# Performance work log

Measured on AMD Instinct MI355X. Metric: run time of the kernel, lower is better.

## Reference

```python
import jax, jax.numpy as jnp
import numpy as np

B, N, D_NODE, D_EDGE, D_GRAPH = 2, 1024, 128, 16, 128
MID, OUT = 64, 128


def _linear_params(key, fan_in, fan_out):
    # haiku Linear default: truncated-normal(stddev=1/sqrt(fan_in)) weight, zero bias
    w = jax.random.normal(key, (fan_in, fan_out), dtype=jnp.float32) / np.sqrt(fan_in)
    b = jnp.zeros((fan_out,), dtype=jnp.float32)
    return w, b


def setup_inputs() -> dict:
    key = jax.random.key(0)
    ks = jax.random.split(key, 12)
    features = jax.random.normal(ks[0], (B, N, D_NODE), dtype=jnp.float32)
    e_features = jax.random.normal(ks[1], (B, N, N, D_EDGE), dtype=jnp.float32)
    g_features = jax.random.normal(ks[2], (B, D_GRAPH), dtype=jnp.float32)
    adj = jax.random.randint(ks[3], (B, N, N), 0, 2).astype(jnp.float32)
    # ensure self-loops so every row has at least one valid neighbor
    adj = jnp.maximum(adj, jnp.eye(N, dtype=jnp.float32)[None])
    Wm, bm = _linear_params(ks[4], D_NODE, OUT)
    Wskip, bskip = _linear_params(ks[5], D_NODE, OUT)
    W1, b1 = _linear_params(ks[6], D_NODE, MID)
    W2, b2 = _linear_params(ks[7], D_NODE, MID)
    We, be = _linear_params(ks[8], D_EDGE, MID)
    Wg, bg = _linear_params(ks[9], D_GRAPH, MID)
    Wa, ba = _linear_params(ks[10], MID, 1)
    return dict(features=features, e_features=e_features, g_features=g_features,
                adj=adj, Wm=Wm, bm=bm, Wskip=Wskip, bskip=bskip,
                W1=W1, b1=b1, W2=W2, b2=b2, We=We, be=be, Wg=Wg, bg=bg,
                Wa=Wa, ba=ba)


def reference(features, e_features, g_features, adj,
              Wm, bm, Wskip, bskip, W1, b1, W2, b2, We, be, Wg, bg, Wa, ba):
    # bias mask: 0 where edge exists, -1e9 where not
    bias_mat = (adj - 1.0) * 1e9  # (b,n,n)

    values = features @ Wm + bm          # (b,n,out)
    pre_att_1 = features @ W1 + b1       # (b,n,mid) -> per-target j
    pre_att_2 = features @ W2 + b2       # (b,n,mid) -> per-source i
    pre_att_e = e_features @ We + be     # (b,n,n,mid)
    pre_att_g = g_features @ Wg + bg     # (b,mid)

    # pre_att[b,i,j] = p1[b,j] + p2[b,i] + pe[b,i,j] + pg[b]
    pre_att = (pre_att_1[:, None, :, :] + pre_att_2[:, :, None, :]
               + pre_att_e + pre_att_g[:, None, None, :])  # (b,n,n,mid)

    logits = jnp.squeeze(jax.nn.leaky_relu(pre_att) @ Wa + ba, axis=-1)  # (b,n,n)
    coefs = jax.nn.softmax(logits + bias_mat, axis=-1)                   # (b,n,n)

    ret = jnp.matmul(coefs, values)       # (b,n,out)
    ret = ret + (features @ Wskip + bskip)  # residual
    return jax.nn.relu(ret)               # activation=relu
```

## Files before the change

kernel.cpp:

```cpp
#include <hip/hip_runtime.h>
#include <hip/hip_bf16.h>
#include <cstdint>

#define B_   2
#define N_   1024
#define DN_  128
#define DE_  16
#define DG_  128
#define MID_ 64
#define OUT_ 128
#define TI_  2
#define PR_ROWS 4

typedef short bf16x8 __attribute__((ext_vector_type(8)));
typedef float f32x4  __attribute__((ext_vector_type(4)));

__device__ inline short f2bf(float f) {
    union { float f; unsigned u; } v; v.f = f;
    unsigned r = v.u + 0x7FFFu + ((v.u >> 16) & 1u);
    return (short)(unsigned short)(r >> 16);
}

__device__ inline unsigned pk2(float lo, float hi) {
    union { __hip_bfloat162 h; unsigned u; } p;
    p.h = __float22bfloat162_rn(make_float2(lo, hi));
    return p.u;
}

__global__ void __launch_bounds__(384) prep_all(
    const float* __restrict__ features, const float* __restrict__ g_features,
    const float* __restrict__ Wm, const float* __restrict__ bm,
    const float* __restrict__ Wskip, const float* __restrict__ bskip,
    const float* __restrict__ W1, const float* __restrict__ b1,
    const float* __restrict__ W2, const float* __restrict__ b2,
    const float* __restrict__ We, const float* __restrict__ be,
    const float* __restrict__ Wg, const float* __restrict__ bg,
    float* __restrict__ values, float* __restrict__ skipo,
    float* __restrict__ P1xT, float* __restrict__ p2,
    float* __restrict__ pg, short* __restrict__ We_frag)
{
    const int t   = threadIdx.x;
    const int blk = blockIdx.x;

    if (blk == 512) {
        for (int e = t; e < 4 * 64 * 8; e += 384) {
            const int c    = e >> 9;
            const int lane = (e >> 3) & 63;
            const int j    = e & 7;
            const int quad = lane >> 4, s = lane & 15;
            short v = 0;
            if (quad < 2) v = f2bf(We[(quad * 8 + j) * MID_ + c * 16 + s]);
            We_frag[e] = v;
        }
        return;
    }
    if (blk == 513) {
        if (t < MID_) {
            float a0 = bg[t], a1 = bg[t];
            for (int k = 0; k < DG_; ++k) {
                const float w = Wg[k * MID_ + t];
                a0 += g_features[k] * w;
                a1 += g_features[DG_ + k] * w;
            }
            pg[t] = a0; pg[MID_ + t] = a1;
        }
        return;
    }

    const int r0 = blk * PR_ROWS;
    __shared__ float feat[PR_ROWS][DN_];
    for (int idx = t; idx < PR_ROWS * DN_; idx += 384)
        feat[idx >> 7][idx & 127] = features[(size_t)r0 * DN_ + idx];
    __syncthreads();

    const float* W; int c, stride; float base; float* outp; int ostride;
    if (t < 128) {
        W = Wm;    c = t;       stride = OUT_; base = bm[c];
        outp = values + (size_t)r0 * OUT_ + c; ostride = OUT_;
    } else if (t < 256) {
        W = Wskip; c = t - 128; stride = OUT_; base = bskip[c];
        outp = skipo + (size_t)r0 * OUT_ + c;  ostride = OUT_;
    } else if (t < 320) {
        W = W1;    c = t - 256; stride = MID_; base = b1[c] + be[c];
        outp = P1xT + (size_t)c * (B_ * N_) + r0; ostride = 1;
    } else {
        W = W2;    c = t - 320; stride = MID_; base = b2[c];
        outp = p2 + (size_t)r0 * MID_ + c;     ostride = MID_;
    }

    float acc[PR_ROWS] = {};
    for (int k = 0; k < DN_; ++k) {
        const float w = W[k * stride + c];
        #pragma unroll
        for (int q = 0; q < PR_ROWS; ++q) acc[q] += feat[q][k] * w;
    }
    #pragma unroll
    for (int q = 0; q < PR_ROWS; ++q) outp[q * ostride] = acc[q] + base;
}

__global__ void __launch_bounds__(256) k_logits(
    const float* __restrict__ e_features, const short* __restrict__ We_frag,
    const float* __restrict__ Wa, const float* __restrict__ P1xT,
    const float* __restrict__ p2, const float* __restrict__ pg,
    float* __restrict__ lg)
{
    const int t    = threadIdx.x;
    const int wv   = t >> 6;
    const int l    = t & 63;
    const int quad = l >> 4;
    const int s    = l & 15;
    const int r    = blockIdx.x;
    const int jb   = r & 1;
    const int ri   = r >> 1;
    const int b    = ri >> 9;
    const int i0   = (ri & 511) * TI_;

    bf16x8 bfr[4];
    float  wa_l[4][4];
    f32x4  p2l[TI_][4];
    #pragma unroll
    for (int c = 0; c < 4; ++c) {
        bfr[c] = *(const bf16x8*)&We_frag[(c * 64 + l) * 8];
        #pragma unroll
        for (int rr = 0; rr < 4; ++rr)
            wa_l[c][rr] = Wa[c * 16 + quad * 4 + rr];
        const float4 pg4 = *(const float4*)&pg[b * MID_ + c * 16 + quad * 4];
        #pragma unroll
        for (int ii = 0; ii < TI_; ++ii) {
            const float4 p4 = *(const float4*)&p2[((size_t)(b * N_ + i0 + ii)) * MID_ + c * 16 + quad * 4];
            p2l[ii][c][0] = p4.x + pg4.x;
            p2l[ii][c][1] = p4.y + pg4.y;
            p2l[ii][c][2] = p4.z + pg4.z;
            p2l[ii][c][3] = p4.w + pg4.w;
        }
    }
    const size_t erow0 = (size_t)(b * N_ + i0) * N_;
    const int jt0 = jb * 32;
    const float* p1b = P1xT + (size_t)(quad * 4) * (B_ * N_) + b * N_ + s;

    float4 eA0[TI_][2], eA1[TI_][2];
    float  bA[4][4], bB[4][4];
    if (quad < 2) {
        #pragma unroll
        for (int ii = 0; ii < TI_; ++ii) {
            const float* ep0 = &e_features[(erow0 + (size_t)ii * N_ + (jt0 + wv) * 16 + s) * DE_ + quad * 8];
            eA0[ii][0] = *(const float4*)ep0;
            eA0[ii][1] = *(const float4*)(ep0 + 4);
            const float* ep1 = &e_features[(erow0 + (size_t)ii * N_ + (jt0 + wv + 4) * 16 + s) * DE_ + quad * 8];
            eA1[ii][0] = *(const float4*)ep1;
            eA1[ii][1] = *(const float4*)(ep1 + 4);
        }
    }
    {
        const float* pb = p1b + (jt0 + wv) * 16;
        #pragma unroll
        for (int c = 0; c < 4; ++c)
            #pragma unroll
            for (int rr = 0; rr < 4; ++rr)
                bA[c][rr] = pb[(size_t)(c * 16 + rr) * (B_ * N_)];
    }

    auto do_tile = [&](float4 (&eAr)[TI_][2], float (&bC)[4][4], float (&bN)[4][4], int it) {
        const int tile = jt0 + wv + it * 4;
        const int j0   = tile * 16;

        unsigned af[TI_][4];
        #pragma unroll
        for (int ii = 0; ii < TI_; ++ii) {
            if (quad < 2) {
                af[ii][0] = pk2(eAr[ii][0].x, eAr[ii][0].y);
                af[ii][1] = pk2(eAr[ii][0].z, eAr[ii][0].w);
                af[ii][2] = pk2(eAr[ii][1].x, eAr[ii][1].y);
                af[ii][3] = pk2(eAr[ii][1].z, eAr[ii][1].w);
            } else {
                af[ii][0] = af[ii][1] = af[ii][2] = af[ii][3] = 0u;
            }
        }
        if (it < 6 && quad < 2) {
            #pragma unroll
            for (int ii = 0; ii < TI_; ++ii) {
                const float* ep = &e_features[(erow0 + (size_t)ii * N_ + (size_t)(tile + 8) * 16 + s) * DE_ + quad * 8];
                eAr[ii][0] = *(const float4*)ep;
                eAr[ii][1] = *(const float4*)(ep + 4);
            }
        }
        if (it < 7) {
            const float* pb = p1b + (tile + 4) * 16;
            #pragma unroll
            for (int c = 0; c < 4; ++c)
                #pragma unroll
                for (int rr = 0; rr < 4; ++rr)
                    bN[c][rr] = pb[(size_t)(c * 16 + rr) * (B_ * N_)];
        }
        #pragma unroll
        for (int ii = 0; ii < TI_; ++ii) {
            union { unsigned u[4]; bf16x8 v; } a;
            a.u[0] = af[ii][0]; a.u[1] = af[ii][1];
            a.u[2] = af[ii][2]; a.u[3] = af[ii][3];
            f32x4 acc[4];
            #pragma unroll
            for (int c = 0; c < 4; ++c)
                acc[c] = __builtin_amdgcn_mfma_f32_16x16x32_bf16(bfr[c], a.v, p2l[ii][c], 0, 0, 0);
            float part = 0.f;
            #pragma unroll
            for (int c = 0; c < 4; ++c)
                #pragma unroll
                for (int rr = 0; rr < 4; ++rr) {
                    float x = acc[c][rr] + bC[c][rr];
                    x = fmaxf(x, 0.01f * x);
                    part += x * wa_l[c][rr];
                }
            part += __shfl_xor(part, 16);
            part += __shfl_xor(part, 32);
            if (l < 16)
                lg[((size_t)(b * N_ + i0 + ii)) * N_ + j0 + l] = part;
        }
    };
    for (int it2 = 0; it2 < 8; it2 += 2) {
        do_tile(eA0, bA, bB, it2);
        do_tile(eA1, bB, bA, it2 + 1);
    }
}

__global__ void __launch_bounds__(256) k_attn(
    const float* __restrict__ lg, const float* __restrict__ adj,
    const float* __restrict__ values, const float* __restrict__ skipo,
    float* __restrict__ out)
{
    const int t  = threadIdx.x;
    const int wv = t >> 6;
    const int l  = t & 63;
    const int r  = blockIdx.x;
    const int b  = (r >> 2) & 1;
    const int i0 = (((r >> 3) << 2) | (r & 3)) * TI_;

    __shared__ float lgP[TI_][N_];
    __shared__ float redv[4][16][20];
    __shared__ float sinv[TI_];
    __shared__ float pmax[4];
    __shared__ float psum[4];

    {
        const int rw = wv & 1, h = wv >> 1;
        const int c0 = h * 512 + l * 4;
        const float* lrow = &lg[(size_t)(b * N_ + i0 + rw) * N_];
        const size_t arb  = (size_t)(b * N_ + i0 + rw) * N_;
        float4 lv[2], av[2];
        #pragma unroll
        for (int q = 0; q < 2; ++q) {
            lv[q] = *(const float4*)&lrow[c0 + 256 * q];
            av[q] = *(const float4*)&adj[arb + c0 + 256 * q];
        }
        const float NEG = -3.4e38f;
        float m = NEG;
        #pragma unroll
        for (int q = 0; q < 2; ++q) {
            m = fmaxf(m, av[q].x > 0.f ? lv[q].x : NEG);
            m = fmaxf(m, av[q].y > 0.f ? lv[q].y : NEG);
            m = fmaxf(m, av[q].z > 0.f ? lv[q].z : NEG);
            m = fmaxf(m, av[q].w > 0.f ? lv[q].w : NEG);
        }
        #pragma unroll
        for (int o = 1; o < 64; o <<= 1) m = fmaxf(m, __shfl_xor(m, o));
        if (l == 0) pmax[wv] = m;
        __syncthreads();
        m = fmaxf(pmax[rw], pmax[2 + rw]);
        float sum = 0.f;
        #pragma unroll
        for (int q = 0; q < 2; ++q) {
            float4 e4;
            e4.x = av[q].x > 0.f ? __expf(lv[q].x - m) : 0.f;
            e4.y = av[q].y > 0.f ? __expf(lv[q].y - m) : 0.f;
            e4.z = av[q].z > 0.f ? __expf(lv[q].z - m) : 0.f;
            e4.w = av[q].w > 0.f ? __expf(lv[q].w - m) : 0.f;
            *(float4*)&lgP[rw][c0 + 256 * q] = e4;
            sum += (e4.x + e4.y) + (e4.z + e4.w);
        }
        #pragma unroll
        for (int o = 1; o < 64; o <<= 1) sum += __shfl_xor(sum, o);
        if (l == 0) psum[wv] = sum;
        __syncthreads();
        if (t < TI_) sinv[t] = 1.0f / (psum[t] + psum[t + 2]);
    }

    const int cg = l & 15, jp = l >> 4, ch0 = cg * 8;
    float acc[TI_][8] = {};
    const float* vb = values + (size_t)b * N_ * OUT_ + ch0;
    for (int k = 0; k < 64; ++k) {
        const int j = wv * 4 + jp + k * 16;
        float cw[TI_];
        #pragma unroll
        for (int ii = 0; ii < TI_; ++ii) cw[ii] = lgP[ii][j];
        const float* vp = vb + (size_t)j * OUT_;
        const float4 v0 = *(const float4*)vp;
        const float4 v1 = *(const float4*)(vp + 4);
        const float vv[8] = {v0.x, v0.y, v0.z, v0.w, v1.x, v1.y, v1.z, v1.w};
        #pragma unroll
        for (int ii = 0; ii < TI_; ++ii)
            #pragma unroll
            for (int kk = 0; kk < 8; ++kk)
                acc[ii][kk] += cw[ii] * vv[kk];
    }
    #pragma unroll
    for (int ii = 0; ii < TI_; ++ii)
        #pragma unroll
        for (int kk = 0; kk < 8; ++kk) {
            acc[ii][kk] += __shfl_xor(acc[ii][kk], 16);
            acc[ii][kk] += __shfl_xor(acc[ii][kk], 32);
        }
    if (l < 16) {
        #pragma unroll
        for (int ii = 0; ii < TI_; ++ii)
            #pragma unroll
            for (int q = 0; q < 2; ++q) {
                float4 w4 = make_float4(acc[ii][q * 4], acc[ii][q * 4 + 1],
                                        acc[ii][q * 4 + 2], acc[ii][q * 4 + 3]);
                *(float4*)&redv[wv][l][ii * 8 + q * 4] = w4;
            }
    }
    __syncthreads();
    {
        const int ch = t & 127, g = ch >> 3, kk = ch & 7;
        const int ii = t >> 7;
        float sum = redv[0][g][ii * 8 + kk];
        #pragma unroll
        for (int w = 1; w < 4; ++w) sum += redv[w][g][ii * 8 + kk];
        const size_t ob = ((size_t)(b * N_ + i0 + ii)) * OUT_ + ch;
        out[ob] = fmaxf(sum * sinv[ii] + skipo[ob], 0.f);
    }
}

extern "C" void kernel_launch(void* const* d_in, const int* in_sizes, int n_in,
                              void* d_out, int out_size, void* d_ws, size_t ws_size,
                              hipStream_t stream) {
    const float* features   = (const float*)d_in[0];
    const float* e_features = (const float*)d_in[1];
    const float* g_features = (const float*)d_in[2];
    const float* adj        = (const float*)d_in[3];
    const float* Wm    = (const float*)d_in[4];
    const float* bm    = (const float*)d_in[5];
    const float* Wskip = (const float*)d_in[6];
    const float* bskip = (const float*)d_in[7];
    const float* W1    = (const float*)d_in[8];
    const float* b1    = (const float*)d_in[9];
    const float* W2    = (const float*)d_in[10];
    const float* b2    = (const float*)d_in[11];
    const float* We    = (const float*)d_in[12];
    const float* be    = (const float*)d_in[13];
    const float* Wg    = (const float*)d_in[14];
    const float* bg    = (const float*)d_in[15];
    const float* Wa    = (const float*)d_in[16];
    float* out = (float*)d_out;

    float* ws      = (float*)d_ws;
    float* values  = ws;
    float* skipo   = ws + 262144;
    float* P1xT    = ws + 524288;
    float* p2      = ws + 655360;
    float* pg      = ws + 786432;
    short* We_frag = (short*)(ws + 786560);
    float* lg      = ws + 787584;

    prep_all<<<B_ * N_ / PR_ROWS + 2, 384, 0, stream>>>(
        features, g_features, Wm, bm, Wskip, bskip, W1, b1, W2, b2,
        We, be, Wg, bg, values, skipo, P1xT, p2, pg, We_frag);
    k_logits<<<B_ * N_ / TI_ * 2, 256, 0, stream>>>(
        e_features, We_frag, Wa, P1xT, p2, pg, lg);
    k_attn<<<B_ * N_ / TI_, 256, 0, stream>>>(
        lg, adj, values, skipo, out);
}
```

Baseline: 294.9 us.

## Store P1 row-major for vector loads and triple-buffer edge feature prefetch

```diff
diff --git a/kernel.cpp b/kernel.cpp
--- a/kernel.cpp
+++ b/kernel.cpp
@@ -36,7 +36,7 @@
     const float* __restrict__ We, const float* __restrict__ be,
     const float* __restrict__ Wg, const float* __restrict__ bg,
     float* __restrict__ values, float* __restrict__ skipo,
-    float* __restrict__ P1xT, float* __restrict__ p2,
+    float* __restrict__ P1x, float* __restrict__ p2,
     float* __restrict__ pg, short* __restrict__ We_frag)
 {
     const int t   = threadIdx.x;
@@ -82,7 +82,7 @@
         outp = skipo + (size_t)r0 * OUT_ + c;  ostride = OUT_;
     } else if (t < 320) {
         W = W1;    c = t - 256; stride = MID_; base = b1[c] + be[c];
-        outp = P1xT + (size_t)c * (B_ * N_) + r0; ostride = 1;
+        outp = P1x + (size_t)r0 * MID_ + c;    ostride = MID_;
     } else {
         W = W2;    c = t - 320; stride = MID_; base = b2[c];
         outp = p2 + (size_t)r0 * MID_ + c;     ostride = MID_;
@@ -100,7 +100,7 @@
 
 __global__ void __launch_bounds__(256) k_logits(
     const float* __restrict__ e_features, const short* __restrict__ We_frag,
-    const float* __restrict__ Wa, const float* __restrict__ P1xT,
+    const float* __restrict__ Wa, const float* __restrict__ P1x,
     const float* __restrict__ p2, const float* __restrict__ pg,
     float* __restrict__ lg)
 {
@@ -116,14 +116,12 @@
     const int i0   = (ri & 511) * TI_;
 
     bf16x8 bfr[4];
-    float  wa_l[4][4];
+    float4 wa4[4];
     f32x4  p2l[TI_][4];
     #pragma unroll
     for (int c = 0; c < 4; ++c) {
         bfr[c] = *(const bf16x8*)&We_frag[(c * 64 + l) * 8];
-        #pragma unroll
-        for (int rr = 0; rr < 4; ++rr)
-            wa_l[c][rr] = Wa[c * 16 + quad * 4 + rr];
+        wa4[c] = *(const float4*)&Wa[c * 16 + quad * 4];
         const float4 pg4 = *(const float4*)&pg[b * MID_ + c * 16 + quad * 4];
         #pragma unroll
         for (int ii = 0; ii < TI_; ++ii) {
@@ -136,31 +134,36 @@
     }
     const size_t erow0 = (size_t)(b * N_ + i0) * N_;
     const int jt0 = jb * 32;
-    const float* p1b = P1xT + (size_t)(quad * 4) * (B_ * N_) + b * N_ + s;
-
-    float4 eA0[TI_][2], eA1[TI_][2];
-    float  bA[4][4], bB[4][4];
-    if (quad < 2) {
-        #pragma unroll
-        for (int ii = 0; ii < TI_; ++ii) {
-            const float* ep0 = &e_features[(erow0 + (size_t)ii * N_ + (jt0 + wv) * 16 + s) * DE_ + quad * 8];
-            eA0[ii][0] = *(const float4*)ep0;
-            eA0[ii][1] = *(const float4*)(ep0 + 4);
-            const float* ep1 = &e_features[(erow0 + (size_t)ii * N_ + (jt0 + wv + 4) * 16 + s) * DE_ + quad * 8];
-            eA1[ii][0] = *(const float4*)ep1;
-            eA1[ii][1] = *(const float4*)(ep1 + 4);
-        }
-    }
-    {
-        const float* pb = p1b + (jt0 + wv) * 16;
-        #pragma unroll
-        for (int c = 0; c < 4; ++c)
-            #pragma unroll
-            for (int rr = 0; rr < 4; ++rr)
-                bA[c][rr] = pb[(size_t)(c * 16 + rr) * (B_ * N_)];
-    }
-
-    auto do_tile = [&](float4 (&eAr)[TI_][2], float (&bC)[4][4], float (&bN)[4][4], int it) {
+
+    float4 eB[3][TI_][2];
+    float  bb[2][4][4];
+
+    auto loadE = [&](float4 (&dst)[TI_][2], int tile) {
+        if (quad < 2) {
+            #pragma unroll
+            for (int ii = 0; ii < TI_; ++ii) {
+                const float* ep = &e_features[(erow0 + (size_t)ii * N_ + (size_t)tile * 16 + s) * DE_ + quad * 8];
+                dst[ii][0] = *(const float4*)ep;
+                dst[ii][1] = *(const float4*)(ep + 4);
+            }
+        }
+    };
+    auto loadB = [&](float (&dst)[4][4], int tile) {
+        const float* pb = &P1x[(size_t)(b * N_ + tile * 16 + s) * MID_ + quad * 4];
+        #pragma unroll
+        for (int c = 0; c < 4; ++c) {
+            const float4 v = *(const float4*)(pb + c * 16);
+            dst[c][0] = v.x; dst[c][1] = v.y; dst[c][2] = v.z; dst[c][3] = v.w;
+        }
+    };
+
+    loadE(eB[0], jt0 + wv);
+    loadE(eB[1], jt0 + wv + 4);
+    loadE(eB[2], jt0 + wv + 8);
+    loadB(bb[0], jt0 + wv);
+
+    #pragma unroll
+    for (int it = 0; it < 8; ++it) {
         const int tile = jt0 + wv + it * 4;
         const int j0   = tile * 16;
 
@@ -168,30 +171,17 @@
         #pragma unroll
         for (int ii = 0; ii < TI_; ++ii) {
             if (quad < 2) {
-                af[ii][0] = pk2(eAr[ii][0].x, eAr[ii][0].y);
-                af[ii][1] = pk2(eAr[ii][0].z, eAr[ii][0].w);
-                af[ii][2] = pk2(eAr[ii][1].x, eAr[ii][1].y);
-                af[ii][3] = pk2(eAr[ii][1].z, eAr[ii][1].w);
+                af[ii][0] = pk2(eB[it % 3][ii][0].x, eB[it % 3][ii][0].y);
+                af[ii][1] = pk2(eB[it % 3][ii][0].z, eB[it % 3][ii][0].w);
+                af[ii][2] = pk2(eB[it % 3][ii][1].x, eB[it % 3][ii][1].y);
+                af[ii][3] = pk2(eB[it % 3][ii][1].z, eB[it % 3][ii][1].w);
             } else {
                 af[ii][0] = af[ii][1] = af[ii][2] = af[ii][3] = 0u;
             }
         }
-        if (it < 6 && quad < 2) {
-            #pragma unroll
-            for (int ii = 0; ii < TI_; ++ii) {
-                const float* ep = &e_features[(erow0 + (size_t)ii * N_ + (size_t)(tile + 8) * 16 + s) * DE_ + quad * 8];
-                eAr[ii][0] = *(const float4*)ep;
-                eAr[ii][1] = *(const float4*)(ep + 4);
-            }
-        }
-        if (it < 7) {
-            const float* pb = p1b + (tile + 4) * 16;
-            #pragma unroll
-            for (int c = 0; c < 4; ++c)
-                #pragma unroll
-                for (int rr = 0; rr < 4; ++rr)
-                    bN[c][rr] = pb[(size_t)(c * 16 + rr) * (B_ * N_)];
-        }
+        if (it < 5) loadE(eB[it % 3], tile + 12);
+        if (it < 7) loadB(bb[(it + 1) & 1], tile + 4);
+
         #pragma unroll
         for (int ii = 0; ii < TI_; ++ii) {
             union { unsigned u[4]; bf16x8 v; } a;
@@ -203,22 +193,22 @@
                 acc[c] = __builtin_amdgcn_mfma_f32_16x16x32_bf16(bfr[c], a.v, p2l[ii][c], 0, 0, 0);
             float part = 0.f;
             #pragma unroll
-            for (int c = 0; c < 4; ++c)
+            for (int c = 0; c < 4; ++c) {
                 #pragma unroll
                 for (int rr = 0; rr < 4; ++rr) {
-                    float x = acc[c][rr] + bC[c][rr];
+                    float x = acc[c][rr] + bb[it & 1][c][rr];
                     x = fmaxf(x, 0.01f * x);
-                    part += x * wa_l[c][rr];
+                    part += x * (c == 0 ? (rr == 0 ? wa4[0].x : rr == 1 ? wa4[0].y : rr == 2 ? wa4[0].z : wa4[0].w)
+                               : c == 1 ? (rr == 0 ? wa4[1].x : rr == 1 ? wa4[1].y : rr == 2 ? wa4[1].z : wa4[1].w)
+                               : c == 2 ? (rr == 0 ? wa4[2].x : rr == 1 ? wa4[2].y : rr == 2 ? wa4[2].z : wa4[2].w)
+                                        : (rr == 0 ? wa4[3].x : rr == 1 ? wa4[3].y : rr == 2 ? wa4[3].z : wa4[3].w));
                 }
+            }
             part += __shfl_xor(part, 16);
             part += __shfl_xor(part, 32);
             if (l < 16)
                 lg[((size_t)(b * N_ + i0 + ii)) * N_ + j0 + l] = part;
         }
-    };
-    for (int it2 = 0; it2 < 8; it2 += 2) {
-        do_tile(eA0, bA, bB, it2);
-        do_tile(eA1, bB, bA, it2 + 1);
     }
 }
 
@@ -355,7 +345,7 @@
     float* ws      = (float*)d_ws;
     float* values  = ws;
     float* skipo   = ws + 262144;
-    float* P1xT    = ws + 524288;
+    float* P1x     = ws + 524288;
     float* p2      = ws + 655360;
     float* pg      = ws + 786432;
     short* We_frag = (short*)(ws + 786560);
@@ -363,9 +353,9 @@
 
     prep_all<<<B_ * N_ / PR_ROWS + 2, 384, 0, stream>>>(
         features, g_features, Wm, bm, Wskip, bskip, W1, b1, W2, b2,
-        We, be, Wg, bg, values, skipo, P1xT, p2, pg, We_frag);
+        We, be, Wg, bg, values, skipo, P1x, p2, pg, We_frag);
     k_logits<<<B_ * N_ / TI_ * 2, 256, 0, stream>>>(
-        e_features, We_frag, Wa, P1xT, p2, pg, lg);
+        e_features, We_frag, Wa, P1x, p2, pg, lg);
     k_attn<<<B_ * N_ / TI_, 256, 0, stream>>>(
         lg, adj, values, skipo, out);
 }
```

Result: no change. 298.6 us (+1.3%).
